# Performance work log

Measured on AMD Instinct MI355X. Metric: run time of the kernel, lower is better.

## Reference

```python
import jax, jax.numpy as jnp
import numpy as np

N = 50000
E = 800000
IN, HID, OUT = 64, 128, 64


def sage_conv(x, edge_index, W_l, b_l, W_r):
    # PyG SAGEConv (aggr='mean', root_weight=True):
    #   out = lin_l(mean_{j in N(i)} x_j) + lin_r(x_i)
    src, dst = edge_index[0], edge_index[1]
    msg = x[src]                                   # [E, d] gather
    agg = jax.ops.segment_sum(msg, dst, num_segments=x.shape[0])  # [N, d]
    cnt = jax.ops.segment_sum(jnp.ones((msg.shape[0],), x.dtype), dst,
                              num_segments=x.shape[0])
    mean = agg / jnp.maximum(cnt, 1.0)[:, None]
    return mean @ W_l + b_l + x @ W_r


def setup_inputs() -> dict:
    key = jax.random.key(0)
    ks = jax.random.split(key, 8)
    x = jax.random.normal(ks[0], (N, IN), dtype=jnp.float32)
    edge_index = jax.random.randint(ks[1], (2, E), 0, N, dtype=jnp.int64)
    s1 = 1.0 / np.sqrt(IN)
    s2 = 1.0 / np.sqrt(HID)
    W1_l = jax.random.uniform(ks[2], (IN, HID), jnp.float32, -s1, s1)
    W1_r = jax.random.uniform(ks[3], (IN, HID), jnp.float32, -s1, s1)
    b1 = jax.random.uniform(ks[4], (HID,), jnp.float32, -s1, s1)
    W2_l = jax.random.uniform(ks[5], (HID, OUT), jnp.float32, -s2, s2)
    W2_r = jax.random.uniform(ks[6], (HID, OUT), jnp.float32, -s2, s2)
    b2 = jax.random.uniform(ks[7], (OUT,), jnp.float32, -s2, s2)
    return {"x": x, "edge_index": edge_index,
            "W1_l": W1_l, "b1": b1, "W1_r": W1_r,
            "W2_l": W2_l, "b2": b2, "W2_r": W2_r}


def reference(x, edge_index, W1_l, b1, W1_r, W2_l, b2, W2_r):
    h = jax.nn.relu(sage_conv(x, edge_index, W1_l, b1, W1_r))
    return sage_conv(h, edge_index, W2_l, b2, W2_r)
```

## Files before the change

### kernel.cpp

```cpp
#include <hip/hip_runtime.h>


#define SCAN_B 256

#define FMA4(acc, f, w0, w1, w2, w3)                          \
  acc.x += f.x * w0.x + f.y * w1.x + f.z * w2.x + f.w * w3.x; \
  acc.y += f.x * w0.y + f.y * w1.y + f.z * w2.y + f.w * w3.y; \
  acc.z += f.x * w0.z + f.y * w1.z + f.z * w2.z + f.w * w3.z; \
  acc.w += f.x * w0.w + f.y * w1.w + f.z * w2.w + f.w * w3.w;

__global__ __launch_bounds__(256) void k_hist(const int* __restrict__ dst,
                                              int* __restrict__ deg, int E) {
  int e = blockIdx.x * blockDim.x + threadIdx.x;
  if (e < E) atomicAdd(&deg[dst[e]], 1);
}

__global__ __launch_bounds__(SCAN_B) void k_scan1(const int* __restrict__ deg,
                                                  int* __restrict__ rowptr,
                                                  int* __restrict__ bsum,
                                                  int N) {
  __shared__ int s[SCAN_B];
  int t = threadIdx.x;
  int gid = blockIdx.x * SCAN_B + t;
  int v = (gid < N) ? deg[gid] : 0;
  s[t] = v;
  __syncthreads();
  for (int off = 1; off < SCAN_B; off <<= 1) {
    int add = (t >= off) ? s[t - off] : 0;
    __syncthreads();
    s[t] += add;
    __syncthreads();
  }
  if (gid < N) rowptr[gid] = s[t] - v;
  if (t == SCAN_B - 1) bsum[blockIdx.x] = s[t];
}

__global__ __launch_bounds__(SCAN_B) void k_scan2(int* __restrict__ bsum,
                                                  int* __restrict__ rowptr,
                                                  int NB, int N) {
  __shared__ int s[SCAN_B];
  int t = threadIdx.x;
  int v = (t < NB) ? bsum[t] : 0;
  s[t] = v;
  __syncthreads();
  for (int off = 1; off < SCAN_B; off <<= 1) {
    int add = (t >= off) ? s[t - off] : 0;
    __syncthreads();
    s[t] += add;
    __syncthreads();
  }
  if (t < NB) bsum[t] = s[t] - v;
  if (t == NB - 1) rowptr[N] = s[t];
}

__global__ __launch_bounds__(SCAN_B) void k_scan3(int* __restrict__ rowptr,
                                                  const int* __restrict__ bsum,
                                                  int* __restrict__ pos,
                                                  int N) {
  int gid = blockIdx.x * SCAN_B + threadIdx.x;
  if (gid < N) {
    int r = rowptr[gid] + bsum[blockIdx.x];
    rowptr[gid] = r;
    pos[gid] = r;
  }
}

__global__ __launch_bounds__(256) void k_fill(const int* __restrict__ src,
                                              const int* __restrict__ dst,
                                              int* __restrict__ pos,
                                              int* __restrict__ colsrc, int E) {
  int e = blockIdx.x * blockDim.x + threadIdx.x;
  if (e >= E) return;
  int slot = atomicAdd(&pos[dst[e]], 1);
  colsrc[slot] = src[e];
}

__global__ __launch_bounds__(256) void k_gather(
    const float* __restrict__ feat, const int* __restrict__ rowptr,
    const int* __restrict__ colsrc, float* __restrict__ mean, int N) {
  int wave = threadIdx.x >> 6;
  int lane = threadIdx.x & 63;
  int node = blockIdx.x * 4 + wave;
  if (node >= N) return;
  int beg = rowptr[node], end = rowptr[node + 1];
  int eg = lane >> 4;
  int c4 = (lane & 15) << 2;
  float4 s = make_float4(0.f, 0.f, 0.f, 0.f);
  for (int e = beg + eg; e < end; e += 4) {
    const float4 v =
        *reinterpret_cast<const float4*>(feat + (size_t)colsrc[e] * 64 + c4);
    s.x += v.x;
    s.y += v.y;
    s.z += v.z;
    s.w += v.w;
  }
#pragma unroll
  for (int m = 16; m <= 32; m <<= 1) {
    s.x += __shfl_xor(s.x, m);
    s.y += __shfl_xor(s.y, m);
    s.z += __shfl_xor(s.z, m);
    s.w += __shfl_xor(s.w, m);
  }
  if (eg == 0) {
    float r = 1.f / fmaxf((float)(end - beg), 1.f);
    float4 o = make_float4(s.x * r, s.y * r, s.z * r, s.w * r);
    *reinterpret_cast<float4*>(mean + (size_t)node * 64 + c4) = o;
  }
}

__global__ __launch_bounds__(256) void k_dense1(
    const float* __restrict__ x, const float* __restrict__ mean1,
    const float* __restrict__ W1l, const float* __restrict__ b1,
    const float* __restrict__ W1r, const float* __restrict__ W2l,
    const float* __restrict__ W2r, float* __restrict__ p,
    float* __restrict__ q, int N) {
  int i0 = blockIdx.x * 32;
  int tid = threadIdx.x;
  __shared__ float ms[32][64];
  __shared__ float xs[32][64];
  __shared__ float hs[32][132];

  for (int t = tid; t < 512; t += 256) {
    int n = t >> 4;
    int c4 = (t & 15) << 2;
    int node = i0 + n;
    float4 zm, zx;
    if (node < N) {
      zm = *(const float4*)&mean1[(size_t)node * 64 + c4];
      zx = *(const float4*)&x[(size_t)node * 64 + c4];
    } else {
      zm = make_float4(0.f, 0.f, 0.f, 0.f);
      zx = zm;
    }
    *(float4*)&ms[n][c4] = zm;
    *(float4*)&xs[n][c4] = zx;
  }
  __syncthreads();

  int jt = tid & 31;
  int j0 = jt << 2;
  int nt = tid >> 5;
  int n0 = nt << 2;
  float4 acc[4];
  {
    float4 bj = *(const float4*)&b1[j0];
    acc[0] = bj; acc[1] = bj; acc[2] = bj; acc[3] = bj;
  }
  for (int k0 = 0; k0 < 64; k0 += 4) {
    float4 wl[4], wr[4];
#pragma unroll
    for (int kk = 0; kk < 4; ++kk) {
      wl[kk] = *(const float4*)&W1l[(size_t)(k0 + kk) * 128 + j0];
      wr[kk] = *(const float4*)&W1r[(size_t)(k0 + kk) * 128 + j0];
    }
#pragma unroll
    for (int n = 0; n < 4; ++n) {
      float4 m4 = *(const float4*)&ms[n0 + n][k0];
      float4 x4 = *(const float4*)&xs[n0 + n][k0];
      FMA4(acc[n], m4, wl[0], wl[1], wl[2], wl[3]);
      FMA4(acc[n], x4, wr[0], wr[1], wr[2], wr[3]);
    }
  }
#pragma unroll
  for (int n = 0; n < 4; ++n) {
    float4 v = acc[n];
    v.x = fmaxf(v.x, 0.f);
    v.y = fmaxf(v.y, 0.f);
    v.z = fmaxf(v.z, 0.f);
    v.w = fmaxf(v.w, 0.f);
    *(float4*)&hs[n0 + n][j0] = v;
  }
  __syncthreads();

  const float* W = (tid < 128) ? W2l : W2r;
  float* ob = (tid < 128) ? p : q;
  int t2 = tid & 127;
  int jt2 = t2 & 15;
  int jj0 = jt2 << 2;
  int nt2 = t2 >> 4;
  int nn0 = nt2 << 2;
  float4 pa[4];
  pa[0] = make_float4(0.f, 0.f, 0.f, 0.f);
  pa[1] = pa[0]; pa[2] = pa[0]; pa[3] = pa[0];
  for (int k0 = 0; k0 < 128; k0 += 4) {
    float4 w[4];
#pragma unroll
    for (int kk = 0; kk < 4; ++kk)
      w[kk] = *(const float4*)&W[(size_t)(k0 + kk) * 64 + jj0];
#pragma unroll
    for (int n = 0; n < 4; ++n) {
      float4 h4 = *(const float4*)&hs[nn0 + n][k0];
      FMA4(pa[n], h4, w[0], w[1], w[2], w[3]);
    }
  }
#pragma unroll
  for (int n = 0; n < 4; ++n) {
    int node = i0 + nn0 + n;
    if (node < N) *(float4*)&ob[(size_t)node * 64 + jj0] = pa[n];
  }
}

__global__ __launch_bounds__(256) void k_final(const float* __restrict__ mean2,
                                               const float* __restrict__ q,
                                               const float* __restrict__ b2,
                                               float* __restrict__ out,
                                               int total4) {
  int i = blockIdx.x * blockDim.x + threadIdx.x;
  if (i >= total4) return;
  float4 m = *(const float4*)&mean2[(size_t)i * 4];
  float4 qq = *(const float4*)&q[(size_t)i * 4];
  float4 b = *(const float4*)&b2[(i & 15) << 2];
  float4 o = make_float4(m.x + qq.x + b.x, m.y + qq.y + b.y,
                         m.z + qq.z + b.z, m.w + qq.w + b.w);
  *(float4*)&out[(size_t)i * 4] = o;
}

extern "C" void kernel_launch(void* const* d_in, const int* in_sizes, int n_in,
                              void* d_out, int out_size, void* d_ws,
                              size_t ws_size, hipStream_t stream) {
  const float* x = (const float*)d_in[0];
  const int* ei = (const int*)d_in[1];
  const float* W1l = (const float*)d_in[2];
  const float* b1 = (const float*)d_in[3];
  const float* W1r = (const float*)d_in[4];
  const float* W2l = (const float*)d_in[5];
  const float* b2 = (const float*)d_in[6];
  const float* W2r = (const float*)d_in[7];
  float* out = (float*)d_out;

  const int N = in_sizes[0] / 64;
  const int E = in_sizes[1] / 2;
  const int* src = ei;
  const int* dst = ei + E;

  int* deg = (int*)d_ws;
  int* rowptr = deg + N;
  int* pos = rowptr + (N + 1);
  int* bsum = pos + N;
  int* colsrc = bsum + 256;
  float* mean = (float*)(colsrc + E);
  float* p = mean + (size_t)N * 64;
  float* q = p + (size_t)N * 64;

  const int NB = (N + SCAN_B - 1) / SCAN_B;

  hipMemsetAsync(deg, 0, (size_t)N * sizeof(int), stream);
  k_hist<<<(E + 255) / 256, 256, 0, stream>>>(dst, deg, E);
  k_scan1<<<NB, SCAN_B, 0, stream>>>(deg, rowptr, bsum, N);
  k_scan2<<<1, SCAN_B, 0, stream>>>(bsum, rowptr, NB, N);
  k_scan3<<<NB, SCAN_B, 0, stream>>>(rowptr, bsum, pos, N);
  k_fill<<<(E + 255) / 256, 256, 0, stream>>>(src, dst, pos, colsrc, E);

  int nblk4 = (N + 3) / 4;
  int nblk32 = (N + 31) / 32;
  k_gather<<<nblk4, 256, 0, stream>>>(x, rowptr, colsrc, mean, N);
  k_dense1<<<nblk32, 256, 0, stream>>>(x, mean, W1l, b1, W1r, W2l, W2r, p, q,
                                       N);
  k_gather<<<nblk4, 256, 0, stream>>>(p, rowptr, colsrc, mean, N);
  int total4 = N * 16;
  k_final<<<(total4 + 255) / 256, 256, 0, stream>>>(mean, q, b2, out, total4);
}
```

Measured before the change: 321.1 us.

## Replace scan with atomic bucket assignment, fuse final add into gather, unroll gather

Replaces the three-kernel prefix scan with one kernel that hands out each node's CSR segment start through an atomicAdd on a global counter, so segments are contiguous but no longer in node order. The second gather now adds q and the bias and writes the output directly, which removes the separate final kernel and one round trip of the N x 64 intermediate. The gather loop is unrolled by two with split accumulators to keep more loads in flight, and dense1 reuses one shared buffer for its inputs and hidden tile, adding a barrier. Atomic segment placement loses locality between node order and edge order, and the contended atomic counter may serialise.

```diff
diff --git a/kernel.cpp b/kernel.cpp
--- a/kernel.cpp
+++ b/kernel.cpp
@@ -1,7 +1,5 @@
 #include <hip/hip_runtime.h>
 
-
-#define SCAN_B 256
 
 #define FMA4(acc, f, w0, w1, w2, w3)                          \
   acc.x += f.x * w0.x + f.y * w1.x + f.z * w2.x + f.w * w3.x; \
@@ -15,54 +13,16 @@
   if (e < E) atomicAdd(&deg[dst[e]], 1);
 }
 
-__global__ __launch_bounds__(SCAN_B) void k_scan1(const int* __restrict__ deg,
-                                                  int* __restrict__ rowptr,
-                                                  int* __restrict__ bsum,
-                                                  int N) {
-  __shared__ int s[SCAN_B];
-  int t = threadIdx.x;
-  int gid = blockIdx.x * SCAN_B + t;
-  int v = (gid < N) ? deg[gid] : 0;
-  s[t] = v;
-  __syncthreads();
-  for (int off = 1; off < SCAN_B; off <<= 1) {
-    int add = (t >= off) ? s[t - off] : 0;
-    __syncthreads();
-    s[t] += add;
-    __syncthreads();
-  }
-  if (gid < N) rowptr[gid] = s[t] - v;
-  if (t == SCAN_B - 1) bsum[blockIdx.x] = s[t];
-}
-
-__global__ __launch_bounds__(SCAN_B) void k_scan2(int* __restrict__ bsum,
-                                                  int* __restrict__ rowptr,
-                                                  int NB, int N) {
-  __shared__ int s[SCAN_B];
-  int t = threadIdx.x;
-  int v = (t < NB) ? bsum[t] : 0;
-  s[t] = v;
-  __syncthreads();
-  for (int off = 1; off < SCAN_B; off <<= 1) {
-    int add = (t >= off) ? s[t - off] : 0;
-    __syncthreads();
-    s[t] += add;
-    __syncthreads();
-  }
-  if (t < NB) bsum[t] = s[t] - v;
-  if (t == NB - 1) rowptr[N] = s[t];
-}
-
-__global__ __launch_bounds__(SCAN_B) void k_scan3(int* __restrict__ rowptr,
-                                                  const int* __restrict__ bsum,
-                                                  int* __restrict__ pos,
-                                                  int N) {
-  int gid = blockIdx.x * SCAN_B + threadIdx.x;
-  if (gid < N) {
-    int r = rowptr[gid] + bsum[blockIdx.x];
-    rowptr[gid] = r;
-    pos[gid] = r;
-  }
+__global__ __launch_bounds__(256) void k_assign(const int* __restrict__ deg,
+                                                int* __restrict__ rowptr,
+                                                int* __restrict__ pos,
+                                                int* __restrict__ total,
+                                                int N) {
+  int i = blockIdx.x * blockDim.x + threadIdx.x;
+  if (i >= N) return;
+  int r = atomicAdd(total, deg[i]);
+  rowptr[i] = r;
+  pos[i] = r;
 }
 
 __global__ __launch_bounds__(256) void k_fill(const int* __restrict__ src,
@@ -77,34 +37,54 @@
 
 __global__ __launch_bounds__(256) void k_gather(
     const float* __restrict__ feat, const int* __restrict__ rowptr,
-    const int* __restrict__ colsrc, float* __restrict__ mean, int N) {
+    const int* __restrict__ deg, const int* __restrict__ colsrc,
+    const float* __restrict__ addsrc, const float* __restrict__ bias,
+    float* __restrict__ dstbuf, int N) {
   int wave = threadIdx.x >> 6;
   int lane = threadIdx.x & 63;
   int node = blockIdx.x * 4 + wave;
   if (node >= N) return;
-  int beg = rowptr[node], end = rowptr[node + 1];
+  int beg = rowptr[node];
+  int d = deg[node];
+  int end = beg + d;
   int eg = lane >> 4;
   int c4 = (lane & 15) << 2;
-  float4 s = make_float4(0.f, 0.f, 0.f, 0.f);
-  for (int e = beg + eg; e < end; e += 4) {
+  float4 s0 = make_float4(0.f, 0.f, 0.f, 0.f);
+  float4 s1 = s0;
+  int e = beg + eg;
+  for (; e + 4 < end; e += 8) {
+    const float4 v0 =
+        *reinterpret_cast<const float4*>(feat + (size_t)colsrc[e] * 64 + c4);
+    const float4 v1 = *reinterpret_cast<const float4*>(
+        feat + (size_t)colsrc[e + 4] * 64 + c4);
+    s0.x += v0.x; s0.y += v0.y; s0.z += v0.z; s0.w += v0.w;
+    s1.x += v1.x; s1.y += v1.y; s1.z += v1.z; s1.w += v1.w;
+  }
+  for (; e < end; e += 4) {
     const float4 v =
         *reinterpret_cast<const float4*>(feat + (size_t)colsrc[e] * 64 + c4);
-    s.x += v.x;
-    s.y += v.y;
-    s.z += v.z;
-    s.w += v.w;
-  }
+    s0.x += v.x; s0.y += v.y; s0.z += v.z; s0.w += v.w;
+  }
+  s0.x += s1.x; s0.y += s1.y; s0.z += s1.z; s0.w += s1.w;
 #pragma unroll
   for (int m = 16; m <= 32; m <<= 1) {
-    s.x += __shfl_xor(s.x, m);
-    s.y += __shfl_xor(s.y, m);
-    s.z += __shfl_xor(s.z, m);
-    s.w += __shfl_xor(s.w, m);
+    s0.x += __shfl_xor(s0.x, m);
+    s0.y += __shfl_xor(s0.y, m);
+    s0.z += __shfl_xor(s0.z, m);
+    s0.w += __shfl_xor(s0.w, m);
   }
   if (eg == 0) {
-    float r = 1.f / fmaxf((float)(end - beg), 1.f);
-    float4 o = make_float4(s.x * r, s.y * r, s.z * r, s.w * r);
-    *reinterpret_cast<float4*>(mean + (size_t)node * 64 + c4) = o;
+    float r = 1.f / fmaxf((float)d, 1.f);
+    float4 o = make_float4(s0.x * r, s0.y * r, s0.z * r, s0.w * r);
+    if (addsrc != nullptr) {
+      float4 a = *(const float4*)&addsrc[(size_t)node * 64 + c4];
+      float4 b = *(const float4*)&bias[c4];
+      o.x += a.x + b.x;
+      o.y += a.y + b.y;
+      o.z += a.z + b.z;
+      o.w += a.w + b.w;
+    }
+    *reinterpret_cast<float4*>(dstbuf + (size_t)node * 64 + c4) = o;
   }
 }
 
@@ -116,9 +96,10 @@
     float* __restrict__ q, int N) {
   int i0 = blockIdx.x * 32;
   int tid = threadIdx.x;
-  __shared__ float ms[32][64];
-  __shared__ float xs[32][64];
-  __shared__ float hs[32][132];
+  __shared__ float smem[32 * 132];
+  float(*ms)[64] = (float(*)[64])smem;
+  float(*xs)[64] = (float(*)[64])(smem + 32 * 64);
+  float(*hs)[132] = (float(*)[132])smem;
 
   for (int t = tid; t < 512; t += 256) {
     int n = t >> 4;
@@ -161,6 +142,8 @@
       FMA4(acc[n], x4, wr[0], wr[1], wr[2], wr[3]);
     }
   }
+  __syncthreads();
+
 #pragma unroll
   for (int n = 0; n < 4; ++n) {
     float4 v = acc[n];
@@ -175,10 +158,8 @@
   const float* W = (tid < 128) ? W2l : W2r;
   float* ob = (tid < 128) ? p : q;
   int t2 = tid & 127;
-  int jt2 = t2 & 15;
-  int jj0 = jt2 << 2;
-  int nt2 = t2 >> 4;
-  int nn0 = nt2 << 2;
+  int jj0 = (t2 & 15) << 2;
+  int nn0 = (t2 >> 4) << 2;
   float4 pa[4];
   pa[0] = make_float4(0.f, 0.f, 0.f, 0.f);
   pa[1] = pa[0]; pa[2] = pa[0]; pa[3] = pa[0];
@@ -198,21 +179,6 @@
     int node = i0 + nn0 + n;
     if (node < N) *(float4*)&ob[(size_t)node * 64 + jj0] = pa[n];
   }
-}
-
-__global__ __launch_bounds__(256) void k_final(const float* __restrict__ mean2,
-                                               const float* __restrict__ q,
-                                               const float* __restrict__ b2,
-                                               float* __restrict__ out,
-                                               int total4) {
-  int i = blockIdx.x * blockDim.x + threadIdx.x;
-  if (i >= total4) return;
-  float4 m = *(const float4*)&mean2[(size_t)i * 4];
-  float4 qq = *(const float4*)&q[(size_t)i * 4];
-  float4 b = *(const float4*)&b2[(i & 15) << 2];
-  float4 o = make_float4(m.x + qq.x + b.x, m.y + qq.y + b.y,
-                         m.z + qq.z + b.z, m.w + qq.w + b.w);
-  *(float4*)&out[(size_t)i * 4] = o;
 }
 
 extern "C" void kernel_launch(void* const* d_in, const int* in_sizes, int n_in,
@@ -234,29 +200,24 @@
   const int* dst = ei + E;
 
   int* deg = (int*)d_ws;
-  int* rowptr = deg + N;
-  int* pos = rowptr + (N + 1);
-  int* bsum = pos + N;
-  int* colsrc = bsum + 256;
+  int* total = deg + N;
+  int* rowptr = total + 1;
+  int* pos = rowptr + N;
+  int* colsrc = pos + N;
   float* mean = (float*)(colsrc + E);
   float* p = mean + (size_t)N * 64;
   float* q = p + (size_t)N * 64;
 
-  const int NB = (N + SCAN_B - 1) / SCAN_B;
-
-  hipMemsetAsync(deg, 0, (size_t)N * sizeof(int), stream);
+  hipMemsetAsync(deg, 0, (size_t)(N + 1) * sizeof(int), stream);
   k_hist<<<(E + 255) / 256, 256, 0, stream>>>(dst, deg, E);
-  k_scan1<<<NB, SCAN_B, 0, stream>>>(deg, rowptr, bsum, N);
-  k_scan2<<<1, SCAN_B, 0, stream>>>(bsum, rowptr, NB, N);
-  k_scan3<<<NB, SCAN_B, 0, stream>>>(rowptr, bsum, pos, N);
+  k_assign<<<(N + 255) / 256, 256, 0, stream>>>(deg, rowptr, pos, total, N);
   k_fill<<<(E + 255) / 256, 256, 0, stream>>>(src, dst, pos, colsrc, E);
 
   int nblk4 = (N + 3) / 4;
   int nblk32 = (N + 31) / 32;
-  k_gather<<<nblk4, 256, 0, stream>>>(x, rowptr, colsrc, mean, N);
+  k_gather<<<nblk4, 256, 0, stream>>>(x, rowptr, deg, colsrc, nullptr, nullptr,
+                                      mean, N);
   k_dense1<<<nblk32, 256, 0, stream>>>(x, mean, W1l, b1, W1r, W2l, W2r, p, q,
                                        N);
-  k_gather<<<nblk4, 256, 0, stream>>>(p, rowptr, colsrc, mean, N);
-  int total4 = N * 16;
-  k_final<<<(total4 + 255) / 256, 256, 0, stream>>>(mean, q, b2, out, total4);
-}
+  k_gather<<<nblk4, 256, 0, stream>>>(p, rowptr, deg, colsrc, q, b2, out, N);
+}
```

After: 324.7 us. Within noise of the previous version (+1.1%).
